# Kernel tuning notes

Hardware: AMD Instinct MI355X
Metric: run time of the kernel (lower is better)

The kernel has to match this reference:

```python
import jax, jax.numpy as jnp
import numpy as np

N_HEADS = 16
CHUNK = 128  # chunk size for blocked causal linear attention


def _phi(x):
    # feature map: elu(x) + 1 (strictly positive)
    return jax.nn.elu(x) + 1.0


def setup_inputs() -> dict:
    key = jax.random.key(0)
    ks = jax.random.split(key, 5)
    d = 1024
    scale = (2.0 / (d + d)) ** 0.5  # xavier_uniform-like std
    W = lambda k: jax.random.normal(k, (d, d), jnp.float32) * scale
    return {
        "x": jax.random.normal(ks[0], (4, 4096, d), jnp.float32),
        "Wq": W(ks[1]), "bq": jnp.zeros((d,), jnp.float32),
        "Wk": W(ks[2]), "bk": jnp.zeros((d,), jnp.float32),
        "Wv": W(ks[3]), "bv": jnp.zeros((d,), jnp.float32),
        "Wo": W(ks[4]), "bo": jnp.zeros((d,), jnp.float32),
    }


def reference(x, Wq, bq, Wk, bk, Wv, bv, Wo, bo):
    b, s, dm = x.shape
    h = N_HEADS
    d = dm // h

    def proj(W, bias):
        # (b, s, dm) -> (b*h, s, d)
        y = x @ W.T + bias
        return y.reshape(b, s, h, d).transpose(0, 2, 1, 3).reshape(b * h, s, d)

    q = _phi(proj(Wq, bq))
    k = _phi(proj(Wk, bk))
    v = proj(Wv, bv)

    C = CHUNK
    n = s // C
    # (b*h, s, d) -> (n_chunks, b*h, C, d) for scan over chunks
    to_chunks = lambda t: t.reshape(b * h, n, C, d).transpose(1, 0, 2, 3)
    qc, kc, vc = to_chunks(q), to_chunks(k), to_chunks(v)
    mask = jnp.tril(jnp.ones((C, C), bool))  # causal within chunk

    def step(carry, inp):
        S, z = carry  # S: (bh, d, d) running sum of k v^T; z: (bh, d) running sum of k
        qi, ki, vi = inp  # each (bh, C, d)
        scores = jnp.einsum('bqd,bkd->bqk', qi, ki)
        scores = jnp.where(mask, scores, jnp.zeros((), scores.dtype))
        num = jnp.einsum('bqk,bkd->bqd', scores, vi) + jnp.einsum('bqd,bde->bqe', qi, S)
        kcum = jnp.cumsum(ki, axis=1) + z[:, None, :]
        den = jnp.sum(qi * kcum, axis=-1, keepdims=True)
        out = num / den
        S2 = S + jnp.einsum('bkd,bke->bde', ki, vi)
        z2 = z + ki.sum(axis=1)
        return (S2, z2), out

    init = (jnp.zeros((b * h, d, d), x.dtype), jnp.zeros((b * h, d), x.dtype))
    _, outs = jax.lax.scan(step, init, (qc, kc, vc))  # outs: (n, bh, C, d)
    out = outs.transpose(1, 0, 2, 3).reshape(b, h, s, d).transpose(0, 2, 1, 3).reshape(b, s, dm)
    return out @ Wo.T + bo
```

## Files before the change

kernel.cpp:

```cpp
#include <hip/hip_runtime.h>
#include <hip/hip_bf16.h>

typedef __attribute__((ext_vector_type(8))) short bf16x8;
typedef __attribute__((ext_vector_type(4))) short bf16x4;
typedef __attribute__((ext_vector_type(4))) float floatx4;
typedef unsigned short u16;
typedef unsigned int u32;

#define DM 1024
#define SEQ 4096
#define NH 16
#define HD 64
#define CHUNK 128

__device__ __forceinline__ float bf2f(u16 x) {
    u32 u = ((u32)x) << 16;
    return __builtin_bit_cast(float, u);
}
__device__ __forceinline__ u16 f2bf(float f) {
    u32 u = __builtin_bit_cast(u32, f);
    u32 r = u + 0x7FFF + ((u >> 16) & 1);
    return (u16)(r >> 16);
}
__device__ __forceinline__ bf16x8 cvt8(const float* p) {
    floatx4 a = *(const floatx4*)p;
    floatx4 b = *(const floatx4*)(p + 4);
    bf16x8 r;
    r[0] = (short)f2bf(a[0]); r[1] = (short)f2bf(a[1]);
    r[2] = (short)f2bf(a[2]); r[3] = (short)f2bf(a[3]);
    r[4] = (short)f2bf(b[0]); r[5] = (short)f2bf(b[1]);
    r[6] = (short)f2bf(b[2]); r[7] = (short)f2bf(b[3]);
    return r;
}
__device__ __forceinline__ void async_copy16(const u16* gsrc, u16* ldst) {
    __builtin_amdgcn_global_load_lds(
        (const __attribute__((address_space(1))) void*)gsrc,
        (__attribute__((address_space(3))) void*)ldst, 16, 0, 0);
}

__global__ void cvt_w_k(const float* __restrict__ Wq, const float* __restrict__ Wk,
                        const float* __restrict__ Wv, const float* __restrict__ Wo,
                        u16* __restrict__ Wqkv, u16* __restrict__ Wob)
{
    int g = blockIdx.x * 256 + threadIdx.x;
    int w = g >> 17;
    int off = g & 131071;
    const float* src = (w == 0) ? Wq : (w == 1) ? Wk : (w == 2) ? Wv : Wo;
    u16* dst = (w < 3) ? (Wqkv + ((size_t)w << 20)) : Wob;
    *(bf16x8*)&dst[(size_t)off * 8] = cvt8(src + (size_t)off * 8);
}

__global__ void cvt_x_k(const float* __restrict__ xs, u16* __restrict__ xb)
{
    size_t g = (size_t)blockIdx.x * 256 + threadIdx.x;
    *(bf16x8*)&xb[g * 8] = cvt8(xs + g * 8);
}

__global__ __launch_bounds__(256, 2) void qkv_gemm_k(
    const u16* __restrict__ xb, const u16* __restrict__ Wqkv,
    const float* __restrict__ bq, const float* __restrict__ bk,
    const float* __restrict__ bv,
    u16* __restrict__ Qh, u16* __restrict__ Kh, u16* __restrict__ Vh,
    int mblocks)
{
    __shared__ __align__(16) u16 sh[2][128 * 64];
    u16* aSh = sh[0];
    u16* bSh = sh[1];
    int t = threadIdx.x, lane = t & 63, w = t >> 6;
    int q = lane >> 4, ln = lane & 15;
    int wm = (w & 1) * 64, wn = (w >> 1) * 64;
    int bid = blockIdx.x;
    int xcd = bid & 7, local = bid >> 3;
    int mPerX = mblocks >> 3;
    int ml = local % mPerX, nn = local / mPerX;
    int m0 = (xcd * mPerX + ml) * 128, n0 = nn * 128;
    int wgr = t & 192;
    floatx4 acc[4][4] = {};

    for (int k0 = 0; k0 < DM; k0 += 64) {
#pragma unroll
        for (int i = 0; i < 4; ++i) {
            int gi = i * 256 + t;
            int r = gi >> 3;
            int c = (gi & 7) ^ (r & 7);
            async_copy16(xb + (size_t)(m0 + r) * DM + k0 + c * 8,
                         aSh + (size_t)(i * 256 + wgr) * 8);
            async_copy16(Wqkv + (size_t)(n0 + r) * DM + k0 + c * 8,
                         bSh + (size_t)(i * 256 + wgr) * 8);
        }
        __builtin_amdgcn_s_waitcnt(0);
        __syncthreads();
#pragma unroll
        for (int ks = 0; ks < 2; ++ks) {
            int cg = ks * 4 + q;
            bf16x8 af[4], bfv[4];
#pragma unroll
            for (int tm = 0; tm < 4; ++tm) {
                int m = wm + tm * 16 + ln;
                af[tm] = *(const bf16x8*)&aSh[(m * 8 + (cg ^ (m & 7))) * 8];
            }
#pragma unroll
            for (int tn = 0; tn < 4; ++tn) {
                int n = wn + tn * 16 + ln;
                bfv[tn] = *(const bf16x8*)&bSh[(n * 8 + (cg ^ (n & 7))) * 8];
            }
#pragma unroll
            for (int tm = 0; tm < 4; ++tm)
#pragma unroll
                for (int tn = 0; tn < 4; ++tn)
                    acc[tm][tn] = __builtin_amdgcn_mfma_f32_16x16x32_bf16(
                        af[tm], bfv[tn], acc[tm][tn], 0, 0, 0);
        }
        __syncthreads();
    }
    int proj = n0 >> 10, colb = n0 & 1023;
    const float* bias = (proj == 0) ? bq : (proj == 1) ? bk : bv;
    u16* plane = (proj == 0) ? Qh : (proj == 1) ? Kh : Vh;
    u16* cSh = sh[0];
#pragma unroll
    for (int tn = 0; tn < 4; ++tn) {
        int lc = wn + tn * 16 + ln;
        float bb = bias[colb + lc];
        int gr = lc >> 3, lo = lc & 7;
#pragma unroll
        for (int tm = 0; tm < 4; ++tm) {
            int lrb = wm + tm * 16 + q * 4;
#pragma unroll
            for (int r = 0; r < 4; ++r) {
                int lr = lrb + r;
                float v = acc[tm][tn][r] + bb;
                if (proj < 2) v = (v > 0.f) ? (v + 1.f) : __expf(v);
                cSh[lr * 128 + ((gr & 8) | ((gr ^ lr) & 7)) * 8 + lo] = f2bf(v);
            }
        }
    }
    __syncthreads();
    int head0 = colb >> 6;
    size_t blk = (size_t)(m0 >> 12);
    int mrow = m0 & 4095;
#pragma unroll
    for (int h = 0; h < 2; ++h) {
        u16* pb = plane + ((blk * NH + head0 + h) * SEQ + mrow) * HD;
#pragma unroll
        for (int it = 0; it < 4; ++it) {
            int gi = it * 256 + t;
            int s = gi >> 3, g = gi & 7;
            *(bf16x8*)&pb[(size_t)gi * 8] =
                *(const bf16x8*)&cSh[s * 128 + ((h * 8) | (g ^ (s & 7))) * 8];
        }
    }
}

__global__ __launch_bounds__(256, 2) void out_gemm_k(
    const u16* __restrict__ Ah, const u16* __restrict__ Wob,
    const float* __restrict__ bo, float* __restrict__ out, int mblocks)
{
    __shared__ __align__(16) u16 aSh[128 * 64];
    __shared__ __align__(16) u16 bSh[128 * 64];
    int t = threadIdx.x, lane = t & 63, w = t >> 6;
    int q = lane >> 4, ln = lane & 15;
    int wm = (w & 1) * 64, wn = (w >> 1) * 64;
    int bid = blockIdx.x;
    int xcd = bid & 7, local = bid >> 3;
    int mPerX = mblocks >> 3;
    int ml = local % mPerX, nn = local / mPerX;
    int m0 = (xcd * mPerX + ml) * 128, n0 = nn * 128;
    int wgr = t & 192;
    floatx4 acc[4][4] = {};

    for (int k0 = 0; k0 < DM; k0 += 64) {
#pragma unroll
        for (int i = 0; i < 4; ++i) {
            int gi = i * 256 + t;
            int r = gi >> 3;
            int c = (gi & 7) ^ (r & 7);
            int rr = m0 + r;
            async_copy16(Ah + (((size_t)((rr >> 12) * NH + (k0 >> 6))) << 18)
                            + (size_t)((rr & 4095) << 6) + (size_t)(c * 8),
                         aSh + (size_t)(i * 256 + wgr) * 8);
            async_copy16(Wob + (size_t)(n0 + r) * DM + k0 + c * 8,
                         bSh + (size_t)(i * 256 + wgr) * 8);
        }
        __builtin_amdgcn_s_waitcnt(0);
        __syncthreads();
#pragma unroll
        for (int ks = 0; ks < 2; ++ks) {
            int cg = ks * 4 + q;
            bf16x8 af[4], bfv[4];
#pragma unroll
            for (int tm = 0; tm < 4; ++tm) {
                int m = wm + tm * 16 + ln;
                af[tm] = *(const bf16x8*)&aSh[(m * 8 + (cg ^ (m & 7))) * 8];
            }
#pragma unroll
            for (int tn = 0; tn < 4; ++tn) {
                int n = wn + tn * 16 + ln;
                bfv[tn] = *(const bf16x8*)&bSh[(n * 8 + (cg ^ (n & 7))) * 8];
            }
#pragma unroll
            for (int tm = 0; tm < 4; ++tm)
#pragma unroll
                for (int tn = 0; tn < 4; ++tn)
                    acc[tm][tn] = __builtin_amdgcn_mfma_f32_16x16x32_bf16(
                        af[tm], bfv[tn], acc[tm][tn], 0, 0, 0);
        }
        __syncthreads();
    }
#pragma unroll
    for (int tn = 0; tn < 4; ++tn) {
        int gn = n0 + wn + tn * 16 + ln;
        float bb = bo[gn];
#pragma unroll
        for (int tm = 0; tm < 4; ++tm) {
            int gmb = m0 + wm + tm * 16 + q * 4;
#pragma unroll
            for (int r = 0; r < 4; ++r)
                out[(size_t)(gmb + r) * DM + gn] = acc[tm][tn][r] + bb;
        }
    }
}

__global__ __launch_bounds__(256, 1) void chunk_stats_k(
    const u16* __restrict__ Kh, const u16* __restrict__ Vh,
    u16* __restrict__ Sc, float* __restrict__ Zc)
{
    __shared__ __align__(16) u16 kSh[128 * 64];
    __shared__ __align__(16) u16 vSh[128 * 64];
    __shared__ float zpart[4][64];
    int t = threadIdx.x;
    int bhc = blockIdx.x;
    const u16* Kb = Kh + ((size_t)(bhc >> 5) * SEQ + (size_t)(bhc & 31) * CHUNK) * HD;
    const u16* Vb = Vh + ((size_t)(bhc >> 5) * SEQ + (size_t)(bhc & 31) * CHUNK) * HD;
#pragma unroll
    for (int i = 0; i < 4; ++i) {
        int g = i * 256 + t;
        *(bf16x8*)&kSh[g * 8] = *(const bf16x8*)&Kb[(size_t)g * 8];
        *(bf16x8*)&vSh[g * 8] = *(const bf16x8*)&Vb[(size_t)g * 8];
    }
    __syncthreads();
    int tD = t & 15, tE = t >> 4;
    float acc[4][4] = {};
#pragma unroll 8
    for (int r = 0; r < 128; ++r) {
        bf16x4 vq = *(const bf16x4*)&vSh[r * 64 + tE * 4];
        bf16x4 kq = *(const bf16x4*)&kSh[r * 64 + tD * 4];
        float vf[4], kf[4];
#pragma unroll
        for (int i = 0; i < 4; ++i) { vf[i] = bf2f((u16)vq[i]); kf[i] = bf2f((u16)kq[i]); }
#pragma unroll
        for (int a = 0; a < 4; ++a)
#pragma unroll
            for (int b = 0; b < 4; ++b) acc[a][b] += vf[a] * kf[b];
    }
    u16* So = Sc + (size_t)bhc * HD * HD;
#pragma unroll
    for (int a = 0; a < 4; ++a) {
        bf16x4 sv;
#pragma unroll
        for (int b = 0; b < 4; ++b) sv[b] = (short)f2bf(acc[a][b]);
        *(bf16x4*)&So[(tE * 4 + a) * HD + tD * 4] = sv;
    }
    {
        int dz = t & 63, qz = t >> 6;
        float z = 0.f;
#pragma unroll
        for (int r = 0; r < 32; ++r) z += bf2f(kSh[(qz * 32 + r) * 64 + dz]);
        zpart[qz][dz] = z;
    }
    __syncthreads();
    if (t < 64)
        Zc[(size_t)bhc * HD + t] =
            zpart[0][t] + zpart[1][t] + zpart[2][t] + zpart[3][t];
}

__global__ void prefix_k(u16* __restrict__ Sc, float* __restrict__ Zc)
{
    int bh = blockIdx.x, y = blockIdx.y, t = threadIdx.x;
    if (y < 32) {
        size_t base = (size_t)bh * 32 * 4096 + y * 128 + t;
        u16 vals[32];
#pragma unroll
        for (int c = 0; c < 32; ++c) vals[c] = Sc[base + (size_t)c * 4096];
        float run = 0.f;
#pragma unroll
        for (int c = 0; c < 32; ++c) {
            float cur = bf2f(vals[c]);
            Sc[base + (size_t)c * 4096] = f2bf(run);
            run += cur;
        }
    } else if (t < 64) {
        size_t base = (size_t)bh * 32 * 64 + t;
        float zv[32];
#pragma unroll
        for (int c = 0; c < 32; ++c) zv[c] = Zc[base + (size_t)c * 64];
        float run = 0.f;
#pragma unroll
        for (int c = 0; c < 32; ++c) {
            Zc[base + (size_t)c * 64] = run;
            run += zv[c];
        }
    }
}

__global__ __launch_bounds__(256, 1) void attn_out_k(
    const u16* Qh, const u16* __restrict__ Kh,
    const u16* __restrict__ Vh, const u16* __restrict__ Sp,
    const float* __restrict__ Zp, u16* Qw)
{
    __shared__ __align__(16) u16 vtSh[64 * 136];
    __shared__ __align__(16) u16 pSh[128 * 136];
    __shared__ float psum[128];
    __shared__ float qzs[128];
    int t = threadIdx.x, lane = t & 63, w = t >> 6;
    int q = lane >> 4, ln = lane & 15;
    int bhc = blockIdx.x, bh = bhc >> 5, ch = bhc & 31;
    const u16* Qb = Qh + ((size_t)bh * SEQ + (size_t)ch * CHUNK) * HD;
    const u16* Kb = Kh + ((size_t)bh * SEQ + (size_t)ch * CHUNK) * HD;
    const u16* Vb = Vh + ((size_t)bh * SEQ + (size_t)ch * CHUNK) * HD;
    const u16* Spb = Sp + (size_t)bhc * HD * HD;
    const float* Zpb = Zp + (size_t)bhc * HD;

#pragma unroll
    for (int i = 0; i < 4; ++i) {
        int g = i * 256 + t;
        int k = g >> 3, e0 = (g & 7) * 8;
        bf16x8 vv = *(const bf16x8*)&Vb[(size_t)k * HD + e0];
#pragma unroll
        for (int j = 0; j < 8; ++j) vtSh[(e0 + j) * 136 + k] = (u16)vv[j];
    }

    int wm = (w & 1) * 64, wn = (w >> 1) * 64;
    bf16x8 afr[2][4];
#pragma unroll
    for (int ks = 0; ks < 2; ++ks)
#pragma unroll
        for (int tm = 0; tm < 4; ++tm) {
            int m = wm + tm * 16 + ln;
            afr[ks][tm] = *(const bf16x8*)&Qb[(size_t)m * HD + ks * 32 + q * 8];
        }
    floatx4 acc[4][4] = {};
#pragma unroll
    for (int ks = 0; ks < 2; ++ks) {
        bf16x8 bfr[4];
#pragma unroll
        for (int tn = 0; tn < 4; ++tn) {
            int n = wn + tn * 16 + ln;
            bfr[tn] = *(const bf16x8*)&Kb[(size_t)n * HD + ks * 32 + q * 8];
        }
#pragma unroll
        for (int tm = 0; tm < 4; ++tm)
#pragma unroll
            for (int tn = 0; tn < 4; ++tn)
                acc[tm][tn] = __builtin_amdgcn_mfma_f32_16x16x32_bf16(
                    afr[ks][tm], bfr[tn], acc[tm][tn], 0, 0, 0);
    }
#pragma unroll
    for (int tm = 0; tm < 4; ++tm) {
        int rb = wm + tm * 16 + q * 4;
#pragma unroll
        for (int tn = 0; tn < 4; ++tn) {
            int cc = wn + tn * 16 + ln;
#pragma unroll
            for (int r = 0; r < 4; ++r) {
                float v = (cc <= rb + r) ? acc[tm][tn][r] : 0.f;
                pSh[(rb + r) * 136 + cc] = f2bf(v);
            }
        }
    }
    __syncthreads();
    if (t < 128) {
        const u16* prow = &pSh[t * 136];
        float s = 0.f;
#pragma unroll
        for (int i = 0; i < 16; ++i) {
            bf16x8 pv = *(const bf16x8*)&prow[i * 8];
#pragma unroll
            for (int j = 0; j < 8; ++j) s += bf2f((u16)pv[j]);
        }
        psum[t] = s;
    } else {
        int row = t - 128;
        float s = 0.f;
#pragma unroll
        for (int i = 0; i < 8; ++i) {
            bf16x8 qv = *(const bf16x8*)&Qb[(size_t)row * HD + i * 8];
#pragma unroll
            for (int j = 0; j < 8; ++j) s += bf2f((u16)qv[j]) * Zpb[i * 8 + j];
        }
        qzs[row] = s;
    }
    __syncthreads();

    int wn2 = (w >> 1) * 32;
    floatx4 acc2[4][2] = {};
#pragma unroll
    for (int ks = 0; ks < 4; ++ks) {
        bf16x8 ap[4], bv[2];
#pragma unroll
        for (int tm = 0; tm < 4; ++tm) {
            int m = wm + tm * 16 + ln;
            ap[tm] = *(const bf16x8*)&pSh[m * 136 + ks * 32 + q * 8];
        }
#pragma unroll
        for (int tn = 0; tn < 2; ++tn) {
            int n = wn2 + tn * 16 + ln;
            bv[tn] = *(const bf16x8*)&vtSh[n * 136 + ks * 32 + q * 8];
        }
#pragma unroll
        for (int tm = 0; tm < 4; ++tm)
#pragma unroll
            for (int tn = 0; tn < 2; ++tn)
                acc2[tm][tn] = __builtin_amdgcn_mfma_f32_16x16x32_bf16(
                    ap[tm], bv[tn], acc2[tm][tn], 0, 0, 0);
    }
#pragma unroll
    for (int ks = 0; ks < 2; ++ks) {
        bf16x8 bs[2];
#pragma unroll
        for (int tn = 0; tn < 2; ++tn) {
            int n = wn2 + tn * 16 + ln;
            bs[tn] = *(const bf16x8*)&Spb[(size_t)n * HD + ks * 32 + q * 8];
        }
#pragma unroll
        for (int tm = 0; tm < 4; ++tm)
#pragma unroll
            for (int tn = 0; tn < 2; ++tn)
                acc2[tm][tn] = __builtin_amdgcn_mfma_f32_16x16x32_bf16(
                    afr[ks][tm], bs[tn], acc2[tm][tn], 0, 0, 0);
    }
    __syncthreads();
#pragma unroll
    for (int tm = 0; tm < 4; ++tm) {
        int rb = wm + tm * 16 + q * 4;
#pragma unroll
        for (int r = 0; r < 4; ++r) {
            int mrow = rb + r;
            float inv = 1.0f / fmaxf(psum[mrow] + qzs[mrow], 1e-20f);
#pragma unroll
            for (int tn = 0; tn < 2; ++tn) {
                int e = wn2 + tn * 16 + ln;
                pSh[mrow * 72 + e] = f2bf(acc2[tm][tn][r] * inv);
            }
        }
    }
    __syncthreads();
    size_t obase = ((size_t)bh * SEQ + (size_t)ch * CHUNK) * HD;
#pragma unroll
    for (int j = 0; j < 4; ++j) {
        int ci = j * 256 + t;
        *(bf16x8*)&Qw[obase + (size_t)ci * 8] =
            *(const bf16x8*)&pSh[(ci >> 3) * 72 + (ci & 7) * 8];
    }
}

extern "C" void kernel_launch(void* const* d_in, const int* in_sizes, int n_in,
                              void* d_out, int out_size, void* d_ws, size_t ws_size,
                              hipStream_t stream) {
    const float* x  = (const float*)d_in[0];
    const float* Wq = (const float*)d_in[1];
    const float* bq = (const float*)d_in[2];
    const float* Wk = (const float*)d_in[3];
    const float* bk = (const float*)d_in[4];
    const float* Wv = (const float*)d_in[5];
    const float* bv = (const float*)d_in[6];
    const float* Wo = (const float*)d_in[7];
    const float* bo = (const float*)d_in[8];
    float* out = (float*)d_out;

    const size_t PLANE = (size_t)NH * SEQ * HD;
    const size_t FIXED = (3 * (size_t)DM * DM + (size_t)DM * DM) * 2;
    const size_t PER_BATCH = 4 * PLANE * 2 + (size_t)NH * 32 * 4096 * 2
                           + (size_t)NH * 32 * HD * 4;
    if (ws_size < FIXED + PER_BATCH) return;
    int nb = (ws_size >= FIXED + 4 * PER_BATCH) ? 4
           : (ws_size >= FIXED + 2 * PER_BATCH) ? 2 : 1;

    char* p0 = (char*)d_ws;
    u16* Wqkv = (u16*)p0;                       p0 += 3 * (size_t)DM * DM * 2;
    u16* Wob  = (u16*)p0;                       p0 += (size_t)DM * DM * 2;

    cvt_w_k<<<dim3(2048), dim3(256), 0, stream>>>(Wq, Wk, Wv, Wo, Wqkv, Wob);

    for (int b0 = 0; b0 < 4; b0 += nb) {
        char* p = p0;
        u16* xb = (u16*)p;  p += (size_t)nb * PLANE * 2;
        u16* Qh = (u16*)p;  p += (size_t)nb * PLANE * 2;
        u16* Kh = (u16*)p;  p += (size_t)nb * PLANE * 2;
        u16* Vh = (u16*)p;  p += (size_t)nb * PLANE * 2;
        u16* Sc = (u16*)p;  p += (size_t)nb * NH * 32 * 4096 * 2;
        float* Zc = (float*)p;
        const float* xs = x + (size_t)b0 * SEQ * DM;
        int mblocks = nb * 32;

        cvt_x_k<<<dim3(nb * 2048), dim3(256), 0, stream>>>(xs, xb);
        qkv_gemm_k<<<dim3(24 * mblocks), dim3(256), 0, stream>>>(
            xb, Wqkv, bq, bk, bv, Qh, Kh, Vh, mblocks);
        chunk_stats_k<<<dim3(nb * 512), dim3(256), 0, stream>>>(Kh, Vh, Sc, Zc);
        prefix_k<<<dim3(nb * 16, 33), dim3(128), 0, stream>>>(Sc, Zc);
        attn_out_k<<<dim3(nb * 512), dim3(256), 0, stream>>>(Qh, Kh, Vh, Sc, Zc, Qh);
        out_gemm_k<<<dim3(8 * mblocks), dim3(256), 0, stream>>>(
            Qh, Wob, bo, out + (size_t)b0 * SEQ * DM, mblocks);
    }
}
```

Before: 378.9 us.

## Double-buffer LDS tiles in QKV and output GEMMs to overlap loads with MFMA

Both bf16 GEMM kernels switch from a single LDS tile pair to two buffers. Each iteration now issues the async global-to-LDS copies for the next K-step before running the MFMAs on the current buffer. The goal is to hide global load latency behind compute instead of stalling on a full wait every step. The cost is doubled LDS per block (64KB), which could limit occupancy. The explicit s_waitcnt was also removed, so correct ordering now depends on __syncthreads emitting a vmcnt wait.

```diff
diff --git a/kernel.cpp b/kernel.cpp
--- a/kernel.cpp
+++ b/kernel.cpp
@@ -63,9 +63,7 @@
     u16* __restrict__ Qh, u16* __restrict__ Kh, u16* __restrict__ Vh,
     int mblocks)
 {
-    __shared__ __align__(16) u16 sh[2][128 * 64];
-    u16* aSh = sh[0];
-    u16* bSh = sh[1];
+    __shared__ __align__(16) u16 lds[32768];
     int t = threadIdx.x, lane = t & 63, w = t >> 6;
     int q = lane >> 4, ln = lane & 15;
     int wm = (w & 1) * 64, wn = (w >> 1) * 64;
@@ -77,19 +75,29 @@
     int wgr = t & 192;
     floatx4 acc[4][4] = {};
 
-    for (int k0 = 0; k0 < DM; k0 += 64) {
+    auto STAGE = [&](int kk, int buf) {
+        int k0 = kk * 64;
+        u16* aS = lds + buf * 16384;
+        u16* bS = aS + 8192;
 #pragma unroll
         for (int i = 0; i < 4; ++i) {
             int gi = i * 256 + t;
             int r = gi >> 3;
             int c = (gi & 7) ^ (r & 7);
             async_copy16(xb + (size_t)(m0 + r) * DM + k0 + c * 8,
-                         aSh + (size_t)(i * 256 + wgr) * 8);
+                         aS + (size_t)(i * 256 + wgr) * 8);
             async_copy16(Wqkv + (size_t)(n0 + r) * DM + k0 + c * 8,
-                         bSh + (size_t)(i * 256 + wgr) * 8);
-        }
-        __builtin_amdgcn_s_waitcnt(0);
-        __syncthreads();
+                         bS + (size_t)(i * 256 + wgr) * 8);
+        }
+    };
+
+    STAGE(0, 0);
+    __syncthreads();
+    for (int tt = 0; tt < 16; ++tt) {
+        int p = tt & 1;
+        if (tt < 15) STAGE(tt + 1, p ^ 1);
+        const u16* aS = lds + p * 16384;
+        const u16* bS = aS + 8192;
 #pragma unroll
         for (int ks = 0; ks < 2; ++ks) {
             int cg = ks * 4 + q;
@@ -97,12 +105,12 @@
 #pragma unroll
             for (int tm = 0; tm < 4; ++tm) {
                 int m = wm + tm * 16 + ln;
-                af[tm] = *(const bf16x8*)&aSh[(m * 8 + (cg ^ (m & 7))) * 8];
+                af[tm] = *(const bf16x8*)&aS[(m * 8 + (cg ^ (m & 7))) * 8];
             }
 #pragma unroll
             for (int tn = 0; tn < 4; ++tn) {
                 int n = wn + tn * 16 + ln;
-                bfv[tn] = *(const bf16x8*)&bSh[(n * 8 + (cg ^ (n & 7))) * 8];
+                bfv[tn] = *(const bf16x8*)&bS[(n * 8 + (cg ^ (n & 7))) * 8];
             }
 #pragma unroll
             for (int tm = 0; tm < 4; ++tm)
@@ -113,10 +121,11 @@
         }
         __syncthreads();
     }
+
     int proj = n0 >> 10, colb = n0 & 1023;
     const float* bias = (proj == 0) ? bq : (proj == 1) ? bk : bv;
     u16* plane = (proj == 0) ? Qh : (proj == 1) ? Kh : Vh;
-    u16* cSh = sh[0];
+    u16* cSh = lds;
 #pragma unroll
     for (int tn = 0; tn < 4; ++tn) {
         int lc = wn + tn * 16 + ln;
@@ -155,8 +164,7 @@
     const u16* __restrict__ Ah, const u16* __restrict__ Wob,
     const float* __restrict__ bo, float* __restrict__ out, int mblocks)
 {
-    __shared__ __align__(16) u16 aSh[128 * 64];
-    __shared__ __align__(16) u16 bSh[128 * 64];
+    __shared__ __align__(16) u16 lds[32768];
     int t = threadIdx.x, lane = t & 63, w = t >> 6;
     int q = lane >> 4, ln = lane & 15;
     int wm = (w & 1) * 64, wn = (w >> 1) * 64;
@@ -168,7 +176,10 @@
     int wgr = t & 192;
     floatx4 acc[4][4] = {};
 
-    for (int k0 = 0; k0 < DM; k0 += 64) {
+    auto STAGE = [&](int kk, int buf) {
+        int k0 = kk * 64;
+        u16* aS = lds + buf * 16384;
+        u16* bS = aS + 8192;
 #pragma unroll
         for (int i = 0; i < 4; ++i) {
             int gi = i * 256 + t;
@@ -177,12 +188,19 @@
             int rr = m0 + r;
             async_copy16(Ah + (((size_t)((rr >> 12) * NH + (k0 >> 6))) << 18)
                             + (size_t)((rr & 4095) << 6) + (size_t)(c * 8),
-                         aSh + (size_t)(i * 256 + wgr) * 8);
+                         aS + (size_t)(i * 256 + wgr) * 8);
             async_copy16(Wob + (size_t)(n0 + r) * DM + k0 + c * 8,
-                         bSh + (size_t)(i * 256 + wgr) * 8);
-        }
-        __builtin_amdgcn_s_waitcnt(0);
-        __syncthreads();
+                         bS + (size_t)(i * 256 + wgr) * 8);
+        }
+    };
+
+    STAGE(0, 0);
+    __syncthreads();
+    for (int tt = 0; tt < 16; ++tt) {
+        int p = tt & 1;
+        if (tt < 15) STAGE(tt + 1, p ^ 1);
+        const u16* aS = lds + p * 16384;
+        const u16* bS = aS + 8192;
 #pragma unroll
         for (int ks = 0; ks < 2; ++ks) {
             int cg = ks * 4 + q;
@@ -190,12 +208,12 @@
 #pragma unroll
             for (int tm = 0; tm < 4; ++tm) {
                 int m = wm + tm * 16 + ln;
-                af[tm] = *(const bf16x8*)&aSh[(m * 8 + (cg ^ (m & 7))) * 8];
+                af[tm] = *(const bf16x8*)&aS[(m * 8 + (cg ^ (m & 7))) * 8];
             }
 #pragma unroll
             for (int tn = 0; tn < 4; ++tn) {
                 int n = wn + tn * 16 + ln;
-                bfv[tn] = *(const bf16x8*)&bSh[(n * 8 + (cg ^ (n & 7))) * 8];
+                bfv[tn] = *(const bf16x8*)&bS[(n * 8 + (cg ^ (n & 7))) * 8];
             }
 #pragma unroll
             for (int tm = 0; tm < 4; ++tm)
@@ -490,15 +508,15 @@
         u16* Sc = (u16*)p;  p += (size_t)nb * NH * 32 * 4096 * 2;
         float* Zc = (float*)p;
         const float* xs = x + (size_t)b0 * SEQ * DM;
-        int mblocks = nb * 32;
+        int mb128 = nb * 32;
 
         cvt_x_k<<<dim3(nb * 2048), dim3(256), 0, stream>>>(xs, xb);
-        qkv_gemm_k<<<dim3(24 * mblocks), dim3(256), 0, stream>>>(
-            xb, Wqkv, bq, bk, bv, Qh, Kh, Vh, mblocks);
+        qkv_gemm_k<<<dim3(24 * mb128), dim3(256), 0, stream>>>(
+            xb, Wqkv, bq, bk, bv, Qh, Kh, Vh, mb128);
         chunk_stats_k<<<dim3(nb * 512), dim3(256), 0, stream>>>(Kh, Vh, Sc, Zc);
         prefix_k<<<dim3(nb * 16, 33), dim3(128), 0, stream>>>(Sc, Zc);
         attn_out_k<<<dim3(nb * 512), dim3(256), 0, stream>>>(Qh, Kh, Vh, Sc, Zc, Qh);
-        out_gemm_k<<<dim3(8 * mblocks), dim3(256), 0, stream>>>(
-            Qh, Wob, bo, out + (size_t)b0 * SEQ * DM, mblocks);
-    }
-}
+        out_gemm_k<<<dim3(8 * mb128), dim3(256), 0, stream>>>(
+            Qh, Wob, bo, out + (size_t)b0 * SEQ * DM, mb128);
+    }
+}
```

After: 371.8 us. No clear change (-1.9%).
